# Optimization experiments

Measured on AMD Instinct MI355X. Metric: run time of the kernel, lower is better.

## Reference

```python
import jax, jax.numpy as jnp
import numpy as np

NUM_UNITS = 64
IN_FEATURES = 256
OUT_FEATURES = 256


def _uw(x, w):
    # per-unit linear: x [B,U,I], w [U,I,O] -> [B,U,O]
    return jnp.einsum('bui,uio->buo', x, w)


def setup_inputs() -> dict:
    key = jax.random.key(0)
    ks = jax.random.split(key, 8)
    bound = float(np.sqrt(1.0 / OUT_FEATURES))
    U, I, O = NUM_UNITS, IN_FEATURES, OUT_FEATURES
    B = 256
    uni = lambda k, s: jax.random.uniform(k, s, jnp.float32, -bound, bound)
    return {
        'x': jax.random.normal(ks[0], (B, U, I), jnp.float32),
        'w_ir': uni(ks[1], (U, I, O)),
        'w_iz': uni(ks[2], (U, I, O)),
        'w_in': uni(ks[3], (U, I, O)),
        'w_hr': uni(ks[4], (U, O, O)),
        'w_hz': uni(ks[5], (U, O, O)),
        'w_hn': uni(ks[6], (U, O, O)),
        'hidden_init': uni(ks[7], (1, U, O)),
    }


def reference(x, w_ir, w_iz, w_in, w_hr, w_hz, w_hn, hidden_init):
    # hidden initialized by broadcasting hidden_init over batch (first call)
    h = jnp.broadcast_to(hidden_init, (x.shape[0],) + hidden_init.shape[1:])
    r = jax.nn.sigmoid(_uw(x, w_ir) + _uw(h, w_hr))
    z = jax.nn.sigmoid(_uw(x, w_iz) + _uw(h, w_hz))
    n = jnp.tanh(_uw(x, w_in) + r * _uw(h, w_hn))
    return (1.0 - z) * n + z * h
```

## Files before the change

### kernel.cpp

```cpp
#include <hip/hip_runtime.h>
#include <hip/hip_bf16.h>

#define UNITS 64
#define IFEAT 256
#define OFEAT 256

typedef __attribute__((ext_vector_type(8))) short v8s;
typedef __attribute__((ext_vector_type(4))) float v4f;

static __device__ __forceinline__ unsigned int pk2(float a, float b) {
    union { __hip_bfloat162 h; unsigned int u; } c;
    c.h = __float22bfloat162_rn(float2{a, b});
    return c.u;
}

static __device__ __forceinline__ float sigmoid_f(float x) {
    return 1.0f / (1.0f + __expf(-x));
}
static __device__ __forceinline__ float tanh_f(float x) {
    float ax = fabsf(x);
    float e = __expf(-2.0f * ax);
    float t = (1.0f - e) / (1.0f + e);
    return copysignf(t, x);
}

__global__ __launch_bounds__(1024, 1) void gru_fused(
    const float* __restrict__ x,
    const float* __restrict__ wir,
    const float* __restrict__ wiz,
    const float* __restrict__ win,
    const float* __restrict__ whr,
    const float* __restrict__ whz,
    const float* __restrict__ whn,
    const float* __restrict__ hinit,
    float* __restrict__ out) {
    __shared__ unsigned short As[32][128][8];
    __shared__ unsigned short Bs[2][3][4][128][8];
    __shared__ unsigned short Ht[32][8];

    const int bid = blockIdx.x;
    const int idx = bid >> 3;
    const int u   = (bid & 7) * 8 + (idx >> 2);
    const int rem = idx & 3;
    const int b0  = (rem >> 1) * 128;
    const int o0  = (rem & 1) * 128;

    const int t    = threadIdx.x;
    const int lane = t & 63;
    const int wv   = t >> 6;
    const int wm   = wv >> 2;
    const int wn   = wv & 3;
    const int lg   = lane >> 4;
    const int lr   = lane & 15;

    const int bcol = t & 127;
    const int bkq  = (t >> 7) & 3;
    const int gA   = t >> 9;
    const bool hasB = (wv < 8);
    const float* wpAx = (gA == 0) ? wir : wiz;
    const float* wpAh = (gA == 0) ? whr : whz;
    const size_t bgbase = (size_t)u * (IFEAT * OFEAT) + (bkq * 8) * OFEAT + o0 + bcol;

    float rbA[8], rbB[8];

    auto bload = [&](const float* pA, const float* pB, int k7) {
        const size_t off = bgbase + (size_t)k7 * 32 * OFEAT;
#pragma unroll
        for (int j = 0; j < 8; ++j) rbA[j] = pA[off + j * OFEAT];
        if (hasB) {
#pragma unroll
            for (int j = 0; j < 8; ++j) rbB[j] = pB[off + j * OFEAT];
        }
    };
    auto bwrite = [&](int bb) {
        uint4 v;
        v.x = pk2(rbA[0], rbA[1]);
        v.y = pk2(rbA[2], rbA[3]);
        v.z = pk2(rbA[4], rbA[5]);
        v.w = pk2(rbA[6], rbA[7]);
        *(uint4*)&Bs[bb][gA][bkq][bcol][0] = v;
        if (hasB) {
            uint4 w;
            w.x = pk2(rbB[0], rbB[1]);
            w.y = pk2(rbB[2], rbB[3]);
            w.z = pk2(rbB[4], rbB[5]);
            w.w = pk2(rbB[6], rbB[7]);
            *(uint4*)&Bs[bb][2][bkq][bcol][0] = w;
        }
    };

    v4f acc[3][2][2];
    v4f acch[2];
#pragma unroll
    for (int g = 0; g < 3; ++g)
#pragma unroll
        for (int mi = 0; mi < 2; ++mi)
#pragma unroll
            for (int ni = 0; ni < 2; ++ni)
                acc[g][mi][ni] = (v4f){0.f, 0.f, 0.f, 0.f};
    acch[0] = (v4f){0.f, 0.f, 0.f, 0.f};
    acch[1] = (v4f){0.f, 0.f, 0.f, 0.f};

    bload(wpAx, win, 0);
    {
        const int kqA = lane >> 1;
        const int j0  = (lane & 1) * 4;
#pragma unroll
        for (int i = 0; i < 8; ++i) {
            const int row = wv * 8 + i;
            v4f q = *(const v4f*)(x + (size_t)(b0 + row) * (UNITS * IFEAT)
                                    + u * IFEAT + lane * 4);
            uint2 w;
            w.x = pk2(q[0], q[1]);
            w.y = pk2(q[2], q[3]);
            *(uint2*)&As[kqA][(row + kqA) & 127][j0] = w;
        }
    }
    if (t < 32) {
        const float* hp = hinit + u * IFEAT + t * 8;
        v4f q0 = *(const v4f*)hp;
        v4f q1 = *(const v4f*)(hp + 4);
        uint4 w;
        w.x = pk2(q0[0], q0[1]);
        w.y = pk2(q0[2], q0[3]);
        w.z = pk2(q1[0], q1[1]);
        w.w = pk2(q1[2], q1[3]);
        *(uint4*)&Ht[t][0] = w;
    }
    bwrite(0);
    bload(wpAx, win, 1);
    __syncthreads();

#pragma unroll
    for (int s = 0; s < 16; ++s) {
        const int bb = s & 1;
        if (s < 15) bwrite(bb ^ 1);
        if (s < 14) {
            const int ns = s + 2;
            bload(ns < 8 ? wpAx : wpAh, ns < 8 ? win : whn, ns & 7);
        }

        if (s < 8) {
            const int kq0 = s * 4 + lg;
            v8s a0 = *(const v8s*)&As[kq0][((wm * 32 + lr) + kq0) & 127][0];
            v8s a1 = *(const v8s*)&As[kq0][((wm * 32 + 16 + lr) + kq0) & 127][0];
#pragma unroll
            for (int g = 0; g < 3; ++g) {
#pragma unroll
                for (int ni = 0; ni < 2; ++ni) {
                    v8s b = *(const v8s*)&Bs[bb][g][lg][wn * 32 + ni * 16 + lr][0];
                    acc[g][0][ni] = __builtin_amdgcn_mfma_f32_16x16x32_bf16(a0, b, acc[g][0][ni], 0, 0, 0);
                    acc[g][1][ni] = __builtin_amdgcn_mfma_f32_16x16x32_bf16(a1, b, acc[g][1][ni], 0, 0, 0);
                }
            }
        } else {
            const int kq0 = (s - 8) * 4 + lg;
            v8s a0 = *(const v8s*)&Ht[kq0][0];
#pragma unroll
            for (int g = 0; g < 2; ++g) {
#pragma unroll
                for (int ni = 0; ni < 2; ++ni) {
                    v8s b = *(const v8s*)&Bs[bb][g][lg][wn * 32 + ni * 16 + lr][0];
                    acc[g][0][ni] = __builtin_amdgcn_mfma_f32_16x16x32_bf16(a0, b, acc[g][0][ni], 0, 0, 0);
                    acc[g][1][ni] = __builtin_amdgcn_mfma_f32_16x16x32_bf16(a0, b, acc[g][1][ni], 0, 0, 0);
                }
            }
#pragma unroll
            for (int ni = 0; ni < 2; ++ni) {
                v8s b = *(const v8s*)&Bs[bb][2][lg][wn * 32 + ni * 16 + lr][0];
                acch[ni] = __builtin_amdgcn_mfma_f32_16x16x32_bf16(a0, b, acch[ni], 0, 0, 0);
            }
        }

        if (s < 15) __syncthreads();
    }

    float h0v[2];
#pragma unroll
    for (int ni = 0; ni < 2; ++ni)
        h0v[ni] = hinit[u * OFEAT + o0 + wn * 32 + ni * 16 + lr];

    const int obase = o0 + wn * 32 + lr;
    const int rbase = b0 + wm * 32 + lg * 4;
#pragma unroll
    for (int mi = 0; mi < 2; ++mi) {
#pragma unroll
        for (int ni = 0; ni < 2; ++ni) {
            const int o = obase + ni * 16;
#pragma unroll
            for (int jj = 0; jj < 4; ++jj) {
                const int row = rbase + mi * 16 + jj;
                const float r = sigmoid_f(acc[0][mi][ni][jj]);
                const float z = sigmoid_f(acc[1][mi][ni][jj]);
                const float n = tanh_f(acc[2][mi][ni][jj] + r * acch[ni][jj]);
                out[((size_t)row * UNITS + u) * OFEAT + o] = (1.0f - z) * n + z * h0v[ni];
            }
        }
    }
}

extern "C" void kernel_launch(void* const* d_in, const int* in_sizes, int n_in,
                              void* d_out, int out_size, void* d_ws, size_t ws_size,
                              hipStream_t stream) {
    const float* x     = (const float*)d_in[0];
    const float* w_ir  = (const float*)d_in[1];
    const float* w_iz  = (const float*)d_in[2];
    const float* w_in  = (const float*)d_in[3];
    const float* w_hr  = (const float*)d_in[4];
    const float* w_hz  = (const float*)d_in[5];
    const float* w_hn  = (const float*)d_in[6];
    const float* hinit = (const float*)d_in[7];
    float* out = (float*)d_out;

    gru_fused<<<dim3(256), dim3(1024), 0, stream>>>(
        x, w_ir, w_iz, w_in, w_hr, w_hz, w_hn, hinit, out);
}
```

Before: 32.62 us.

## Load weights straight into MFMA B registers, dropping shared-memory B staging

Each block now runs 8 waves instead of 16. Each wave owns a 16-column slice of the output and covers all 128 batch rows. The weight fragments are loaded from global memory straight into registers, converted to bf16, and fed to MFMA without going through shared memory. This removes the LDS B buffers and the per-step __syncthreads, and double-buffers the loads in registers. The trade-offs are more registers per thread, weight loads that may be less coalesced (8 strided rows per lane), and fewer waves to hide memory latency.

```diff
diff --git a/kernel.cpp b/kernel.cpp
--- a/kernel.cpp
+++ b/kernel.cpp
@@ -24,7 +24,7 @@
     return copysignf(t, x);
 }
 
-__global__ __launch_bounds__(1024, 1) void gru_fused(
+__global__ __launch_bounds__(512, 1) void gru_fused(
     const float* __restrict__ x,
     const float* __restrict__ wir,
     const float* __restrict__ wiz,
@@ -35,7 +35,6 @@
     const float* __restrict__ hinit,
     float* __restrict__ out) {
     __shared__ unsigned short As[32][128][8];
-    __shared__ unsigned short Bs[2][3][4][128][8];
     __shared__ unsigned short Ht[32][8];
 
     const int bid = blockIdx.x;
@@ -48,66 +47,18 @@
     const int t    = threadIdx.x;
     const int lane = t & 63;
     const int wv   = t >> 6;
-    const int wm   = wv >> 2;
-    const int wn   = wv & 3;
     const int lg   = lane >> 4;
     const int lr   = lane & 15;
 
-    const int bcol = t & 127;
-    const int bkq  = (t >> 7) & 3;
-    const int gA   = t >> 9;
-    const bool hasB = (wv < 8);
-    const float* wpAx = (gA == 0) ? wir : wiz;
-    const float* wpAh = (gA == 0) ? whr : whz;
-    const size_t bgbase = (size_t)u * (IFEAT * OFEAT) + (bkq * 8) * OFEAT + o0 + bcol;
+    const float* WX[3] = {wir, wiz, win};
+    const float* WH[3] = {whr, whz, whn};
 
-    float rbA[8], rbB[8];
-
-    auto bload = [&](const float* pA, const float* pB, int k7) {
-        const size_t off = bgbase + (size_t)k7 * 32 * OFEAT;
-#pragma unroll
-        for (int j = 0; j < 8; ++j) rbA[j] = pA[off + j * OFEAT];
-        if (hasB) {
-#pragma unroll
-            for (int j = 0; j < 8; ++j) rbB[j] = pB[off + j * OFEAT];
-        }
-    };
-    auto bwrite = [&](int bb) {
-        uint4 v;
-        v.x = pk2(rbA[0], rbA[1]);
-        v.y = pk2(rbA[2], rbA[3]);
-        v.z = pk2(rbA[4], rbA[5]);
-        v.w = pk2(rbA[6], rbA[7]);
-        *(uint4*)&Bs[bb][gA][bkq][bcol][0] = v;
-        if (hasB) {
-            uint4 w;
-            w.x = pk2(rbB[0], rbB[1]);
-            w.y = pk2(rbB[2], rbB[3]);
-            w.z = pk2(rbB[4], rbB[5]);
-            w.w = pk2(rbB[6], rbB[7]);
-            *(uint4*)&Bs[bb][2][bkq][bcol][0] = w;
-        }
-    };
-
-    v4f acc[3][2][2];
-    v4f acch[2];
-#pragma unroll
-    for (int g = 0; g < 3; ++g)
-#pragma unroll
-        for (int mi = 0; mi < 2; ++mi)
-#pragma unroll
-            for (int ni = 0; ni < 2; ++ni)
-                acc[g][mi][ni] = (v4f){0.f, 0.f, 0.f, 0.f};
-    acch[0] = (v4f){0.f, 0.f, 0.f, 0.f};
-    acch[1] = (v4f){0.f, 0.f, 0.f, 0.f};
-
-    bload(wpAx, win, 0);
     {
         const int kqA = lane >> 1;
         const int j0  = (lane & 1) * 4;
 #pragma unroll
-        for (int i = 0; i < 8; ++i) {
-            const int row = wv * 8 + i;
+        for (int i = 0; i < 16; ++i) {
+            const int row = wv * 16 + i;
             v4f q = *(const v4f*)(x + (size_t)(b0 + row) * (UNITS * IFEAT)
                                     + u * IFEAT + lane * 4);
             uint2 w;
@@ -127,74 +78,91 @@
         w.w = pk2(q1[2], q1[3]);
         *(uint4*)&Ht[t][0] = w;
     }
-    bwrite(0);
-    bload(wpAx, win, 1);
+
+    const size_t bcolofs = (size_t)u * (IFEAT * OFEAT) + o0 + wv * 16 + lr;
+
+    float rbA[3][8], rbB[3][8];
+
+#define LOADB(dst, s)                                                        \
+    {                                                                        \
+        const float* const* W = ((s) < 8) ? WX : WH;                         \
+        const size_t boff = bcolofs + (size_t)(((s) & 7) * 4 + lg) * 8 * OFEAT; \
+        _Pragma("unroll")                                                    \
+        for (int g = 0; g < 3; ++g) {                                        \
+            const float* p = W[g] + boff;                                    \
+            _Pragma("unroll")                                                \
+            for (int j = 0; j < 8; ++j) dst[g][j] = p[j * OFEAT];            \
+        }                                                                    \
+    }
+
+    v4f acc[3][8];
+    v4f acch;
+#pragma unroll
+    for (int g = 0; g < 3; ++g)
+#pragma unroll
+        for (int mi = 0; mi < 8; ++mi)
+            acc[g][mi] = (v4f){0.f, 0.f, 0.f, 0.f};
+    acch = (v4f){0.f, 0.f, 0.f, 0.f};
+
+    LOADB(rbA, 0);
     __syncthreads();
 
 #pragma unroll
     for (int s = 0; s < 16; ++s) {
-        const int bb = s & 1;
-        if (s < 15) bwrite(bb ^ 1);
-        if (s < 14) {
-            const int ns = s + 2;
-            bload(ns < 8 ? wpAx : wpAh, ns < 8 ? win : whn, ns & 7);
+        if (s < 15) {
+            if (s & 1) { LOADB(rbA, s + 1); }
+            else       { LOADB(rbB, s + 1); }
+        }
+        const float (*rb)[8] = (s & 1) ? rbB : rbA;
+
+        v8s bf[3];
+#pragma unroll
+        for (int g = 0; g < 3; ++g) {
+            uint4 v;
+            v.x = pk2(rb[g][0], rb[g][1]);
+            v.y = pk2(rb[g][2], rb[g][3]);
+            v.z = pk2(rb[g][4], rb[g][5]);
+            v.w = pk2(rb[g][6], rb[g][7]);
+            union { uint4 u4; v8s s8; } cv;
+            cv.u4 = v;
+            bf[g] = cv.s8;
         }
 
+        const int kq = (s & 7) * 4 + lg;
         if (s < 8) {
-            const int kq0 = s * 4 + lg;
-            v8s a0 = *(const v8s*)&As[kq0][((wm * 32 + lr) + kq0) & 127][0];
-            v8s a1 = *(const v8s*)&As[kq0][((wm * 32 + 16 + lr) + kq0) & 127][0];
 #pragma unroll
-            for (int g = 0; g < 3; ++g) {
+            for (int mi = 0; mi < 8; ++mi) {
+                v8s a = *(const v8s*)&As[kq][((mi * 16 + lr) + kq) & 127][0];
 #pragma unroll
-                for (int ni = 0; ni < 2; ++ni) {
-                    v8s b = *(const v8s*)&Bs[bb][g][lg][wn * 32 + ni * 16 + lr][0];
-                    acc[g][0][ni] = __builtin_amdgcn_mfma_f32_16x16x32_bf16(a0, b, acc[g][0][ni], 0, 0, 0);
-                    acc[g][1][ni] = __builtin_amdgcn_mfma_f32_16x16x32_bf16(a1, b, acc[g][1][ni], 0, 0, 0);
-                }
+                for (int g = 0; g < 3; ++g)
+                    acc[g][mi] = __builtin_amdgcn_mfma_f32_16x16x32_bf16(
+                        a, bf[g], acc[g][mi], 0, 0, 0);
             }
         } else {
-            const int kq0 = (s - 8) * 4 + lg;
-            v8s a0 = *(const v8s*)&Ht[kq0][0];
+            v8s a0h = *(const v8s*)&Ht[kq][0];
 #pragma unroll
-            for (int g = 0; g < 2; ++g) {
+            for (int g = 0; g < 2; ++g)
 #pragma unroll
-                for (int ni = 0; ni < 2; ++ni) {
-                    v8s b = *(const v8s*)&Bs[bb][g][lg][wn * 32 + ni * 16 + lr][0];
-                    acc[g][0][ni] = __builtin_amdgcn_mfma_f32_16x16x32_bf16(a0, b, acc[g][0][ni], 0, 0, 0);
-                    acc[g][1][ni] = __builtin_amdgcn_mfma_f32_16x16x32_bf16(a0, b, acc[g][1][ni], 0, 0, 0);
-                }
-            }
+                for (int mi = 0; mi < 8; ++mi)
+                    acc[g][mi] = __builtin_amdgcn_mfma_f32_16x16x32_bf16(
+                        a0h, bf[g], acc[g][mi], 0, 0, 0);
+            acch = __builtin_amdgcn_mfma_f32_16x16x32_bf16(a0h, bf[2], acch, 0, 0, 0);
+        }
+    }
+#undef LOADB
+
+    const int o = o0 + wv * 16 + lr;
+    const float h0v = hinit[u * OFEAT + o];
 #pragma unroll
-            for (int ni = 0; ni < 2; ++ni) {
-                v8s b = *(const v8s*)&Bs[bb][2][lg][wn * 32 + ni * 16 + lr][0];
-                acch[ni] = __builtin_amdgcn_mfma_f32_16x16x32_bf16(a0, b, acch[ni], 0, 0, 0);
-            }
-        }
-
-        if (s < 15) __syncthreads();
-    }
-
-    float h0v[2];
+    for (int mi = 0; mi < 8; ++mi) {
 #pragma unroll
-    for (int ni = 0; ni < 2; ++ni)
-        h0v[ni] = hinit[u * OFEAT + o0 + wn * 32 + ni * 16 + lr];
-
-    const int obase = o0 + wn * 32 + lr;
-    const int rbase = b0 + wm * 32 + lg * 4;
-#pragma unroll
-    for (int mi = 0; mi < 2; ++mi) {
-#pragma unroll
-        for (int ni = 0; ni < 2; ++ni) {
-            const int o = obase + ni * 16;
-#pragma unroll
-            for (int jj = 0; jj < 4; ++jj) {
-                const int row = rbase + mi * 16 + jj;
-                const float r = sigmoid_f(acc[0][mi][ni][jj]);
-                const float z = sigmoid_f(acc[1][mi][ni][jj]);
-                const float n = tanh_f(acc[2][mi][ni][jj] + r * acch[ni][jj]);
-                out[((size_t)row * UNITS + u) * OFEAT + o] = (1.0f - z) * n + z * h0v[ni];
-            }
+        for (int jj = 0; jj < 4; ++jj) {
+            const int row = b0 + mi * 16 + lg * 4 + jj;
+            const float r = sigmoid_f(acc[0][mi][jj]);
+            const float z = sigmoid_f(acc[1][mi][jj]);
+            const float n = tanh_f(acc[2][mi][jj] + r * acch[jj]);
+            out[(size_t)row * (UNITS * OFEAT) + u * OFEAT + o] =
+                (1.0f - z) * n + z * h0v;
         }
     }
 }
@@ -212,6 +180,6 @@
     const float* hinit = (const float*)d_in[7];
     float* out = (float*)d_out;
 
-    gru_fused<<<dim3(256), dim3(1024), 0, stream>>>(
+    gru_fused<<<dim3(256), dim3(512), 0, stream>>>(
         x, w_ir, w_iz, w_in, w_hr, w_hz, w_hn, hinit, out);
 }
```

Result: no change. 32.47 us (-0.4%).
